# Performance work log

Measured on AMD Instinct MI355X. Metric: run time of the kernel, lower is better.

## Reference

```python
import jax, jax.numpy as jnp
import numpy as np

B, T, D, H, Dh = 2, 2048, 2048, 16, 128


def setup_inputs() -> dict:
    key = jax.random.key(0)
    ks = jax.random.split(key, 9)
    s = 0.02
    return {
        "x": jax.random.normal(ks[0], (B, T, D), jnp.float32),
        "Wq": jax.random.normal(ks[1], (H, D, Dh), jnp.float32) * s,
        "bq": jax.random.normal(ks[2], (H, Dh), jnp.float32) * s,
        "Wk": jax.random.normal(ks[3], (H, D, Dh), jnp.float32) * s,
        "bk": jax.random.normal(ks[4], (H, Dh), jnp.float32) * s,
        "Wv": jax.random.normal(ks[5], (H, D, Dh), jnp.float32) * s,
        "bv": jax.random.normal(ks[6], (H, Dh), jnp.float32) * s,
        "Wp": jax.random.normal(ks[7], (D, D), jnp.float32) * s,
        "bp": jax.random.normal(ks[8], (D,), jnp.float32) * s,
    }


def reference(x, Wq, bq, Wk, bk, Wv, bv, Wp, bp):
    # per-head projections (stacked): [B, H, T, Dh]
    q = jnp.einsum("btd,hde->bhte", x, Wq) + bq[None, :, None, :]
    k = jnp.einsum("btd,hde->bhte", x, Wk) + bk[None, :, None, :]
    v = jnp.einsum("btd,hde->bhte", x, Wv) + bv[None, :, None, :]
    scale = Dh ** -0.5
    att = jnp.einsum("bhte,bhse->bhts", q, k) * scale  # [B,H,T,T]
    causal = jnp.tril(jnp.ones((T, T), bool))
    att = jnp.where(causal, att, -jnp.inf)
    att = jax.nn.softmax(att, axis=-1)
    # dropout p=0.0 -> identity
    out = jnp.einsum("bhts,bhse->bhte", att, v)  # [B,H,T,Dh]
    out = out.transpose(0, 2, 1, 3).reshape(B, T, H * Dh)  # concat heads
    return out @ Wp.T if False else jnp.einsum("btd,ed->bte", out, Wp.T) if False else out @ Wp + bp
```

## Files before the change

kernel.cpp:

```cpp
#include <hip/hip_runtime.h>
#include <hip/hip_bf16.h>
#include <math.h>

typedef __attribute__((ext_vector_type(8))) short bf16x8;
typedef __attribute__((ext_vector_type(8))) unsigned short u16x8;
typedef __attribute__((ext_vector_type(4))) float f32x4;
typedef __attribute__((ext_vector_type(16))) float f32x16;

__device__ __forceinline__ unsigned short f2b(float f) {
    union { float f; unsigned u; } a; a.f = f;
    unsigned r = a.u + 0x7FFFu + ((a.u >> 16) & 1u);
    return (unsigned short)(r >> 16);
}

__device__ __forceinline__ void gl_lds16(const unsigned short* g, unsigned short* l) {
    __builtin_amdgcn_global_load_lds(
        (const __attribute__((address_space(1))) unsigned int*)g,
        (__attribute__((address_space(3))) unsigned int*)l,
        16, 0, 0);
}

#define SCALE2 0.12751744716529944f

__global__ __launch_bounds__(256) void prep_kernel(
    const float* __restrict__ x,
    const float* __restrict__ Wq, const float* __restrict__ Wk,
    const float* __restrict__ Wv, const float* __restrict__ Wp,
    unsigned short* __restrict__ xb, unsigned short* __restrict__ wt,
    unsigned short* __restrict__ wpt) {
    __shared__ float tile_s[64][65];
    int bid = blockIdx.x;
    int t = threadIdx.x;
    if (bid < 4096) {
        const float* src; unsigned short* dst;
        int r0, c0, sstride;
        if (bid < 3072) {
            int z = bid >> 6;
            int tile = bid & 63;
            r0 = (tile >> 1) * 64; c0 = (tile & 1) * 64;
            int mat = z >> 4, hh = z & 15;
            src = ((mat == 0) ? Wq : (mat == 1) ? Wk : Wv) + (size_t)hh * 2048 * 128;
            dst = wt + (size_t)z * 128 * 2048;
            sstride = 128;
        } else {
            int tile = bid - 3072;
            r0 = (tile >> 5) * 64; c0 = (tile & 31) * 64;
            src = Wp; dst = wpt; sstride = 2048;
        }
        int row = t >> 2, q = t & 3;
#pragma unroll
        for (int i = 0; i < 4; ++i) {
            float4 v = *(const float4*)&src[(size_t)(r0 + row) * sstride + c0 + q * 16 + i * 4];
            tile_s[row][q * 16 + i * 4 + 0] = v.x;
            tile_s[row][q * 16 + i * 4 + 1] = v.y;
            tile_s[row][q * 16 + i * 4 + 2] = v.z;
            tile_s[row][q * 16 + i * 4 + 3] = v.w;
        }
        __syncthreads();
#pragma unroll
        for (int half = 0; half < 2; ++half) {
            u16x8 o;
#pragma unroll
            for (int u = 0; u < 8; ++u)
                o[u] = f2b(tile_s[q * 16 + half * 8 + u][row]);
            *(u16x8*)&dst[(size_t)(c0 + row) * 2048 + r0 + q * 16 + half * 8] = o;
        }
    } else {
        size_t idx = (size_t)(bid - 4096) * 256 + t;
        float4 v0 = ((const float4*)x)[idx * 2];
        float4 v1 = ((const float4*)x)[idx * 2 + 1];
        u16x8 o;
        o[0] = f2b(v0.x); o[1] = f2b(v0.y); o[2] = f2b(v0.z); o[3] = f2b(v0.w);
        o[4] = f2b(v1.x); o[5] = f2b(v1.y); o[6] = f2b(v1.z); o[7] = f2b(v1.w);
        ((u16x8*)xb)[idx] = o;
    }
}

constexpr int BKg = 64;

__global__ __launch_bounds__(256) void qkv_gemm_kernel(
    const unsigned short* __restrict__ xb,
    const unsigned short* __restrict__ wt,
    const float* __restrict__ bq, const float* __restrict__ bkb, const float* __restrict__ bvb,
    unsigned short* __restrict__ q, unsigned short* __restrict__ k, unsigned short* __restrict__ vt) {
    __shared__ unsigned short sA[128 * 64];
    __shared__ unsigned short sB[128 * 64];
    int cb = blockIdx.x;
    int m0 = blockIdx.y * 128;
    int tid = threadIdx.x;
    int lane = tid & 63, w = tid >> 6;
    int wm = w >> 1, wn = w & 1;
    int l32 = lane & 31, kh = lane >> 5;
    int srow = lane >> 3;
    int gcol = ((lane & 7) ^ srow) * 8;
    int swz = l32 & 7;

    f32x16 acc[2][2] = {};
    const unsigned short* aBase = xb + (size_t)m0 * 2048;
    const unsigned short* bBase = wt + (size_t)cb * 128 * 2048;

    for (int k0 = 0; k0 < 2048; k0 += BKg) {
#pragma unroll
        for (int p = 0; p < 4; ++p) {
            int row = w * 32 + p * 8 + srow;
            gl_lds16(aBase + (size_t)row * 2048 + k0 + gcol, sA + (w * 32 + p * 8) * 64);
            gl_lds16(bBase + (size_t)row * 2048 + k0 + gcol, sB + (w * 32 + p * 8) * 64);
        }
        __syncthreads();
#pragma unroll
        for (int kst = 0; kst < 4; ++kst) {
            int chunk = kst * 2 + kh;
            bf16x8 af[2], bfr[2];
#pragma unroll
            for (int a = 0; a < 2; ++a)
                af[a] = *(const bf16x8*)(sA + (wm * 64 + a * 32 + l32) * 64 + (chunk ^ swz) * 8);
#pragma unroll
            for (int b = 0; b < 2; ++b)
                bfr[b] = *(const bf16x8*)(sB + (wn * 64 + b * 32 + l32) * 64 + (chunk ^ swz) * 8);
#pragma unroll
            for (int a = 0; a < 2; ++a)
#pragma unroll
                for (int b = 0; b < 2; ++b)
                    acc[a][b] = __builtin_amdgcn_mfma_f32_32x32x16_bf16(af[a], bfr[b], acc[a][b], 0, 0, 0);
        }
        __syncthreads();
    }

    int mat = cb >> 4, h = cb & 15;
    const float* bias = (mat == 0) ? bq : (mat == 1) ? bkb : bvb;
    unsigned short* outqk = (mat == 0) ? q : k;
    float postscale = (mat == 0) ? SCALE2 : 1.0f;
#pragma unroll
    for (int a = 0; a < 2; ++a) {
#pragma unroll
        for (int b = 0; b < 2; ++b) {
            int col = wn * 64 + b * 32 + l32;
            float bb = bias[h * 128 + col];
            if (mat < 2) {
#pragma unroll
                for (int reg = 0; reg < 16; ++reg) {
                    int gr = m0 + wm * 64 + a * 32 + (reg & 3) + 8 * (reg >> 2) + 4 * kh;
                    int bi = gr >> 11, t = gr & 2047;
                    outqk[((size_t)(bi * 16 + h) * 2048 + t) * 128 + col] =
                        f2b((acc[a][b][reg] + bb) * postscale);
                }
            } else {
#pragma unroll
                for (int rg = 0; rg < 4; ++rg) {
                    int gr = m0 + wm * 64 + a * 32 + 8 * rg + 4 * kh;
                    int bi = gr >> 11, t = gr & 2047;
                    ushort4 pk;
                    pk.x = f2b(acc[a][b][rg * 4 + 0] + bb);
                    pk.y = f2b(acc[a][b][rg * 4 + 1] + bb);
                    pk.z = f2b(acc[a][b][rg * 4 + 2] + bb);
                    pk.w = f2b(acc[a][b][rg * 4 + 3] + bb);
                    *(ushort4*)(vt + ((size_t)(bi * 16 + h) * 128 + col) * 2048 + t) = pk;
                }
            }
        }
    }
}

__global__ __launch_bounds__(256) void attn_kernel(
    const unsigned short* __restrict__ qg,
    const unsigned short* __restrict__ kg,
    const unsigned short* __restrict__ vg,
    unsigned short* __restrict__ og) {
    constexpr int LDP = 72;
    __shared__ unsigned short sK[2][64 * 128];
    __shared__ unsigned short sV[2][128 * 64];
    __shared__ unsigned short sP[4 * 16 * LDP];

    int bh = blockIdx.x;
    int t0 = (31 - (int)blockIdx.y) * 64;
    int tid = threadIdx.x;
    int lane = tid & 63, w = tid >> 6;
    int ln = lane & 15, quad = lane >> 4;
    int swz = ln & 7;

    const unsigned short* qb = qg + (size_t)bh * 2048 * 128;
    const unsigned short* kb = kg + (size_t)bh * 2048 * 128;
    const unsigned short* vb = vg + (size_t)bh * 128 * 2048;

    bf16x8 qf[4];
#pragma unroll
    for (int c = 0; c < 4; ++c)
        qf[c] = *(const bf16x8*)(qb + (size_t)(t0 + w * 16 + ln) * 128 + c * 32 + quad * 8);

    f32x4 oacc[8] = {};
    float lst[4] = {0.f, 0.f, 0.f, 0.f};

    int nblk = t0 / 64 + 1;

    int kr = lane >> 4, km = lane & 15;
    int vr = lane >> 3, vm = lane & 7;

    {
        int s0 = 0;
#pragma unroll
        for (int p = 0; p < 4; ++p) {
            int krow = w * 16 + p * 4;
            int rswk = (krow + kr) & 7;
            int kch = (km & 8) | ((km & 7) ^ rswk);
            gl_lds16(kb + (size_t)(s0 + krow + kr) * 128 + kch * 8, sK[0] + krow * 128);
            int vrow = w * 32 + p * 8;
            int vch = vm ^ vr;
            gl_lds16(vb + (size_t)(vrow + vr) * 2048 + s0 + vch * 8, sV[0] + vrow * 64);
        }
    }

    for (int jb = 0; jb < nblk; ++jb) {
        int s0 = jb * 64;
        int buf = jb & 1;
        __syncthreads();
        if (jb + 1 < nblk) {
            int s1 = s0 + 64;
#pragma unroll
            for (int p = 0; p < 4; ++p) {
                int krow = w * 16 + p * 4;
                int rswk = (krow + kr) & 7;
                int kch = (km & 8) | ((km & 7) ^ rswk);
                gl_lds16(kb + (size_t)(s1 + krow + kr) * 128 + kch * 8, sK[buf ^ 1] + krow * 128);
                int vrow = w * 32 + p * 8;
                int vch = vm ^ vr;
                gl_lds16(vb + (size_t)(vrow + vr) * 2048 + s1 + vch * 8, sV[buf ^ 1] + vrow * 64);
            }
        }
        bool diag = (jb == nblk - 1);

        f32x4 sacc[4] = {};
#pragma unroll
        for (int c = 0; c < 4; ++c) {
            bf16x8 bfr[4];
#pragma unroll
            for (int j = 0; j < 4; ++j) {
                int ch = c * 4 + quad;
                int pos = (ch & 8) | ((ch ^ swz) & 7);
                bfr[j] = *(const bf16x8*)(sK[buf] + (j * 16 + ln) * 128 + pos * 8);
            }
#pragma unroll
            for (int j = 0; j < 4; ++j)
                sacc[j] = __builtin_amdgcn_mfma_f32_16x16x32_bf16(qf[c], bfr[j], sacc[j], 0, 0, 0);
        }
#pragma unroll
        for (int r = 0; r < 4; ++r) {
            int t = t0 + w * 16 + quad * 4 + r;
            float p_[4];
#pragma unroll
            for (int j = 0; j < 4; ++j) {
                float e_ = exp2f(sacc[j][r]);
                if (diag && (s0 + j * 16 + ln > t)) e_ = 0.f;
                p_[j] = e_;
                sP[(w * 16 + quad * 4 + r) * LDP + j * 16 + ln] = f2b(e_);
            }
            lst[r] += (p_[0] + p_[1]) + (p_[2] + p_[3]);
        }
#pragma unroll
        for (int c2 = 0; c2 < 2; ++c2) {
            bf16x8 af, bfr[8];
            af = *(const bf16x8*)(sP + (w * 16 + ln) * LDP + c2 * 32 + quad * 8);
#pragma unroll
            for (int jj = 0; jj < 8; ++jj) {
                int pos = (c2 * 4 + quad) ^ swz;
                bfr[jj] = *(const bf16x8*)(sV[buf] + (jj * 16 + ln) * 64 + pos * 8);
            }
#pragma unroll
            for (int jj = 0; jj < 8; ++jj)
                oacc[jj] = __builtin_amdgcn_mfma_f32_16x16x32_bf16(af, bfr[jj], oacc[jj], 0, 0, 0);
        }
    }

#pragma unroll
    for (int r = 0; r < 4; ++r) {
        int t = t0 + w * 16 + quad * 4 + r;
        float lsum = lst[r];
#pragma unroll
        for (int m_ = 8; m_ >= 1; m_ >>= 1)
            lsum += __shfl_xor(lsum, m_, 64);
        float inv = 1.f / lsum;
#pragma unroll
        for (int jj = 0; jj < 8; ++jj) {
            int e = jj * 16 + ln;
            og[((size_t)bh * 2048 + t) * 128 + e] = f2b(oacc[jj][r] * inv);
        }
    }
}

__global__ __launch_bounds__(256) void proj_gemm_kernel(
    const unsigned short* __restrict__ og,
    const unsigned short* __restrict__ wpt,
    const float* __restrict__ bp,
    float* __restrict__ out) {
    __shared__ unsigned short sA[128 * 64];
    __shared__ unsigned short sB[128 * 64];
    int cb = blockIdx.x;
    int m0 = blockIdx.y * 128;
    int b_ = m0 >> 11, t0_ = m0 & 2047;
    int tid = threadIdx.x;
    int lane = tid & 63, w = tid >> 6;
    int wm = w >> 1, wn = w & 1;
    int l32 = lane & 31, kh = lane >> 5;
    int srow = lane >> 3;
    int gcol = ((lane & 7) ^ srow) * 8;
    int swz = l32 & 7;

    f32x16 acc[2][2] = {};
    const unsigned short* bBase = wpt + (size_t)cb * 128 * 2048;

    for (int k0 = 0; k0 < 2048; k0 += BKg) {
        int h = k0 >> 7, e0 = k0 & 127;
        const unsigned short* aBase = og + ((size_t)(b_ * 16 + h) * 2048 + t0_) * 128 + e0;
#pragma unroll
        for (int p = 0; p < 4; ++p) {
            int row = w * 32 + p * 8 + srow;
            gl_lds16(aBase + (size_t)row * 128 + gcol, sA + (w * 32 + p * 8) * 64);
            gl_lds16(bBase + (size_t)row * 2048 + k0 + gcol, sB + (w * 32 + p * 8) * 64);
        }
        __syncthreads();
#pragma unroll
        for (int kst = 0; kst < 4; ++kst) {
            int chunk = kst * 2 + kh;
            bf16x8 af[2], bfr[2];
#pragma unroll
            for (int a = 0; a < 2; ++a)
                af[a] = *(const bf16x8*)(sA + (wm * 64 + a * 32 + l32) * 64 + (chunk ^ swz) * 8);
#pragma unroll
            for (int b = 0; b < 2; ++b)
                bfr[b] = *(const bf16x8*)(sB + (wn * 64 + b * 32 + l32) * 64 + (chunk ^ swz) * 8);
#pragma unroll
            for (int a = 0; a < 2; ++a)
#pragma unroll
                for (int b = 0; b < 2; ++b)
                    acc[a][b] = __builtin_amdgcn_mfma_f32_32x32x16_bf16(af[a], bfr[b], acc[a][b], 0, 0, 0);
        }
        __syncthreads();
    }

#pragma unroll
    for (int a = 0; a < 2; ++a)
#pragma unroll
        for (int b = 0; b < 2; ++b) {
            int col = cb * 128 + wn * 64 + b * 32 + l32;
            float bias = bp[col];
#pragma unroll
            for (int reg = 0; reg < 16; ++reg) {
                int row = m0 + wm * 64 + a * 32 + (reg & 3) + 8 * (reg >> 2) + 4 * kh;
                out[(size_t)row * 2048 + col] = acc[a][b][reg] + bias;
            }
        }
}

extern "C" void kernel_launch(void* const* d_in, const int* in_sizes, int n_in,
                              void* d_out, int out_size, void* d_ws, size_t ws_size,
                              hipStream_t stream) {
    const float* x  = (const float*)d_in[0];
    const float* Wq = (const float*)d_in[1];
    const float* bq = (const float*)d_in[2];
    const float* Wk = (const float*)d_in[3];
    const float* bk = (const float*)d_in[4];
    const float* Wv = (const float*)d_in[5];
    const float* bv = (const float*)d_in[6];
    const float* Wp = (const float*)d_in[7];
    const float* bp = (const float*)d_in[8];
    float* out = (float*)d_out;

    char* ws = (char*)d_ws;
    unsigned short* xb  = (unsigned short*)(ws);
    unsigned short* wt  = (unsigned short*)(ws + 16777216);
    unsigned short* wpt = (unsigned short*)(ws + 41943040);
    unsigned short* q   = (unsigned short*)(ws + 50331648);
    unsigned short* k   = (unsigned short*)(ws + 67108864);
    unsigned short* vt  = (unsigned short*)(ws + 83886080);
    unsigned short* o   = (unsigned short*)(ws + 100663296);

    prep_kernel<<<8192, 256, 0, stream>>>(x, Wq, Wk, Wv, Wp, xb, wt, wpt);
    qkv_gemm_kernel<<<dim3(48, 32), 256, 0, stream>>>(xb, wt, bq, bk, bv, q, k, vt);
    attn_kernel<<<dim3(32, 32), 256, 0, stream>>>(q, k, vt, o);
    proj_gemm_kernel<<<dim3(16, 32), 256, 0, stream>>>(o, wpt, bp, out);
}
```

Measured before the change: 361.7 us.

## Enlarge attention query tile to 128 rows and pair causal tiles per block

```diff
diff --git a/kernel.cpp b/kernel.cpp
--- a/kernel.cpp
+++ b/kernel.cpp
@@ -166,13 +166,12 @@
     const unsigned short* __restrict__ kg,
     const unsigned short* __restrict__ vg,
     unsigned short* __restrict__ og) {
-    constexpr int LDP = 72;
     __shared__ unsigned short sK[2][64 * 128];
     __shared__ unsigned short sV[2][128 * 64];
-    __shared__ unsigned short sP[4 * 16 * LDP];
+    __shared__ unsigned short sP[128 * 64];
 
     int bh = blockIdx.x;
-    int t0 = (31 - (int)blockIdx.y) * 64;
+    int qp = blockIdx.y;
     int tid = threadIdx.x;
     int lane = tid & 63, w = tid >> 6;
     int ln = lane & 15, quad = lane >> 4;
@@ -182,107 +181,123 @@
     const unsigned short* kb = kg + (size_t)bh * 2048 * 128;
     const unsigned short* vb = vg + (size_t)bh * 128 * 2048;
 
-    bf16x8 qf[4];
-#pragma unroll
-    for (int c = 0; c < 4; ++c)
-        qf[c] = *(const bf16x8*)(qb + (size_t)(t0 + w * 16 + ln) * 128 + c * 32 + quad * 8);
-
-    f32x4 oacc[8] = {};
-    float lst[4] = {0.f, 0.f, 0.f, 0.f};
-
-    int nblk = t0 / 64 + 1;
-
     int kr = lane >> 4, km = lane & 15;
     int vr = lane >> 3, vm = lane & 7;
 
-    {
-        int s0 = 0;
+    for (int ph = 0; ph < 2; ++ph) {
+        int Q = ph ? (15 - qp) : qp;
+        int t0 = Q * 128;
+        int nblk = 2 * Q + 2;
+
+        bf16x8 qf[2][4];
+#pragma unroll
+        for (int rg = 0; rg < 2; ++rg)
+#pragma unroll
+            for (int c = 0; c < 4; ++c)
+                qf[rg][c] = *(const bf16x8*)(qb + (size_t)(t0 + w * 32 + rg * 16 + ln) * 128 + c * 32 + quad * 8);
+
+        f32x4 oacc[2][8] = {};
+        float lst[2][4] = {};
+
 #pragma unroll
         for (int p = 0; p < 4; ++p) {
             int krow = w * 16 + p * 4;
             int rswk = (krow + kr) & 7;
             int kch = (km & 8) | ((km & 7) ^ rswk);
-            gl_lds16(kb + (size_t)(s0 + krow + kr) * 128 + kch * 8, sK[0] + krow * 128);
+            gl_lds16(kb + (size_t)(krow + kr) * 128 + kch * 8, sK[0] + krow * 128);
             int vrow = w * 32 + p * 8;
             int vch = vm ^ vr;
-            gl_lds16(vb + (size_t)(vrow + vr) * 2048 + s0 + vch * 8, sV[0] + vrow * 64);
-        }
-    }
-
-    for (int jb = 0; jb < nblk; ++jb) {
-        int s0 = jb * 64;
-        int buf = jb & 1;
-        __syncthreads();
-        if (jb + 1 < nblk) {
-            int s1 = s0 + 64;
-#pragma unroll
-            for (int p = 0; p < 4; ++p) {
-                int krow = w * 16 + p * 4;
-                int rswk = (krow + kr) & 7;
-                int kch = (km & 8) | ((km & 7) ^ rswk);
-                gl_lds16(kb + (size_t)(s1 + krow + kr) * 128 + kch * 8, sK[buf ^ 1] + krow * 128);
-                int vrow = w * 32 + p * 8;
-                int vch = vm ^ vr;
-                gl_lds16(vb + (size_t)(vrow + vr) * 2048 + s1 + vch * 8, sV[buf ^ 1] + vrow * 64);
-            }
-        }
-        bool diag = (jb == nblk - 1);
-
-        f32x4 sacc[4] = {};
-#pragma unroll
-        for (int c = 0; c < 4; ++c) {
-            bf16x8 bfr[4];
-#pragma unroll
-            for (int j = 0; j < 4; ++j) {
-                int ch = c * 4 + quad;
-                int pos = (ch & 8) | ((ch ^ swz) & 7);
-                bfr[j] = *(const bf16x8*)(sK[buf] + (j * 16 + ln) * 128 + pos * 8);
-            }
-#pragma unroll
-            for (int j = 0; j < 4; ++j)
-                sacc[j] = __builtin_amdgcn_mfma_f32_16x16x32_bf16(qf[c], bfr[j], sacc[j], 0, 0, 0);
-        }
-#pragma unroll
-        for (int r = 0; r < 4; ++r) {
-            int t = t0 + w * 16 + quad * 4 + r;
-            float p_[4];
-#pragma unroll
-            for (int j = 0; j < 4; ++j) {
-                float e_ = exp2f(sacc[j][r]);
-                if (diag && (s0 + j * 16 + ln > t)) e_ = 0.f;
-                p_[j] = e_;
-                sP[(w * 16 + quad * 4 + r) * LDP + j * 16 + ln] = f2b(e_);
-            }
-            lst[r] += (p_[0] + p_[1]) + (p_[2] + p_[3]);
-        }
-#pragma unroll
-        for (int c2 = 0; c2 < 2; ++c2) {
-            bf16x8 af, bfr[8];
-            af = *(const bf16x8*)(sP + (w * 16 + ln) * LDP + c2 * 32 + quad * 8);
-#pragma unroll
-            for (int jj = 0; jj < 8; ++jj) {
-                int pos = (c2 * 4 + quad) ^ swz;
-                bfr[jj] = *(const bf16x8*)(sV[buf] + (jj * 16 + ln) * 64 + pos * 8);
-            }
-#pragma unroll
-            for (int jj = 0; jj < 8; ++jj)
-                oacc[jj] = __builtin_amdgcn_mfma_f32_16x16x32_bf16(af, bfr[jj], oacc[jj], 0, 0, 0);
-        }
-    }
-
-#pragma unroll
-    for (int r = 0; r < 4; ++r) {
-        int t = t0 + w * 16 + quad * 4 + r;
-        float lsum = lst[r];
-#pragma unroll
-        for (int m_ = 8; m_ >= 1; m_ >>= 1)
-            lsum += __shfl_xor(lsum, m_, 64);
-        float inv = 1.f / lsum;
-#pragma unroll
-        for (int jj = 0; jj < 8; ++jj) {
-            int e = jj * 16 + ln;
-            og[((size_t)bh * 2048 + t) * 128 + e] = f2b(oacc[jj][r] * inv);
-        }
+            gl_lds16(vb + (size_t)(vrow + vr) * 2048 + vch * 8, sV[0] + vrow * 64);
+        }
+
+        for (int jb = 0; jb < nblk; ++jb) {
+            int s0 = jb * 64;
+            int buf = jb & 1;
+            __syncthreads();
+            if (jb + 1 < nblk) {
+                int s1 = s0 + 64;
+#pragma unroll
+                for (int p = 0; p < 4; ++p) {
+                    int krow = w * 16 + p * 4;
+                    int rswk = (krow + kr) & 7;
+                    int kch = (km & 8) | ((km & 7) ^ rswk);
+                    gl_lds16(kb + (size_t)(s1 + krow + kr) * 128 + kch * 8, sK[buf ^ 1] + krow * 128);
+                    int vrow = w * 32 + p * 8;
+                    int vch = vm ^ vr;
+                    gl_lds16(vb + (size_t)(vrow + vr) * 2048 + s1 + vch * 8, sV[buf ^ 1] + vrow * 64);
+                }
+            }
+            bool diag = (jb >= nblk - 2);
+
+            f32x4 sacc[2][4] = {};
+#pragma unroll
+            for (int c = 0; c < 4; ++c) {
+                bf16x8 bfr[4];
+#pragma unroll
+                for (int j = 0; j < 4; ++j) {
+                    int ch = c * 4 + quad;
+                    int pos = (ch & 8) | ((ch ^ swz) & 7);
+                    bfr[j] = *(const bf16x8*)(sK[buf] + (j * 16 + ln) * 128 + pos * 8);
+                }
+#pragma unroll
+                for (int j = 0; j < 4; ++j)
+#pragma unroll
+                    for (int rg = 0; rg < 2; ++rg)
+                        sacc[rg][j] = __builtin_amdgcn_mfma_f32_16x16x32_bf16(qf[rg][c], bfr[j], sacc[rg][j], 0, 0, 0);
+            }
+#pragma unroll
+            for (int rg = 0; rg < 2; ++rg)
+#pragma unroll
+                for (int r = 0; r < 4; ++r) {
+                    int rr = w * 32 + rg * 16 + quad * 4 + r;
+                    int t = t0 + rr;
+                    int rs = rr & 7;
+                    float p_[4];
+#pragma unroll
+                    for (int j = 0; j < 4; ++j) {
+                        float e_ = exp2f(sacc[rg][j][r]);
+                        if (diag && (s0 + j * 16 + ln > t)) e_ = 0.f;
+                        p_[j] = e_;
+                        int col = j * 16 + ln;
+                        sP[rr * 64 + (((col >> 3) ^ rs) << 3) + (col & 7)] = f2b(e_);
+                    }
+                    lst[rg][r] += (p_[0] + p_[1]) + (p_[2] + p_[3]);
+                }
+#pragma unroll
+            for (int c2 = 0; c2 < 2; ++c2) {
+                bf16x8 pa[2], bfr[8];
+#pragma unroll
+                for (int rg = 0; rg < 2; ++rg)
+                    pa[rg] = *(const bf16x8*)(sP + (w * 32 + rg * 16 + ln) * 64 + (((c2 * 4 + quad) ^ swz) << 3));
+#pragma unroll
+                for (int jj = 0; jj < 8; ++jj) {
+                    int pos = (c2 * 4 + quad) ^ swz;
+                    bfr[jj] = *(const bf16x8*)(sV[buf] + (jj * 16 + ln) * 64 + pos * 8);
+                }
+#pragma unroll
+                for (int jj = 0; jj < 8; ++jj)
+#pragma unroll
+                    for (int rg = 0; rg < 2; ++rg)
+                        oacc[rg][jj] = __builtin_amdgcn_mfma_f32_16x16x32_bf16(pa[rg], bfr[jj], oacc[rg][jj], 0, 0, 0);
+            }
+        }
+
+#pragma unroll
+        for (int rg = 0; rg < 2; ++rg)
+#pragma unroll
+            for (int r = 0; r < 4; ++r) {
+                int t = t0 + w * 32 + rg * 16 + quad * 4 + r;
+                float lsum = lst[rg][r];
+#pragma unroll
+                for (int m_ = 8; m_ >= 1; m_ >>= 1)
+                    lsum += __shfl_xor(lsum, m_, 64);
+                float inv = 1.f / lsum;
+#pragma unroll
+                for (int jj = 0; jj < 8; ++jj) {
+                    int e = jj * 16 + ln;
+                    og[((size_t)bh * 2048 + t) * 128 + e] = f2b(oacc[rg][jj][r] * inv);
+                }
+            }
     }
 }
 
@@ -375,6 +390,6 @@
 
     prep_kernel<<<8192, 256, 0, stream>>>(x, Wq, Wk, Wv, Wp, xb, wt, wpt);
     qkv_gemm_kernel<<<dim3(48, 32), 256, 0, stream>>>(xb, wt, bq, bk, bv, q, k, vt);
-    attn_kernel<<<dim3(32, 32), 256, 0, stream>>>(q, k, vt, o);
+    attn_kernel<<<dim3(32, 8), 256, 0, stream>>>(q, k, vt, o);
     proj_gemm_kernel<<<dim3(16, 32), 256, 0, stream>>>(o, wpt, bp, out);
 }
```

New measurement: 400.0 us. +10.6%, slower.
